# Kernel optimization log

Hardware: AMD Instinct MI355X
Metric: run time of the kernel (lower is better)

The kernel has to match this reference:

```python
import jax, jax.numpy as jnp
import numpy as np

D_MODEL = 1440; D_INNER = 2880; D_STATE = 128; HEADDIM = 64; NHEADS = 45
D_CONV = 4; NLAYERS = 32; VOCAB = 256; CHUNK = 128
D_XBC = D_INNER + 2 * D_STATE          # 3136 conv channels
D_PROJ = 2 * D_INNER + 2 * D_STATE + NHEADS  # 6061 in_proj width
EPS = 1e-5

def silu(x):
    return x * jax.nn.sigmoid(x)

def segsum(x):
    # x: (..., T) -> (..., T, T); out[i, j] = sum_{j < k <= i} x[k], -inf above diagonal
    T = x.shape[-1]
    xe = jnp.broadcast_to(x[..., None], (*x.shape, T))
    lower = jnp.tril(jnp.ones((T, T), bool), -1)
    cs = jnp.cumsum(jnp.where(lower, xe, 0.0), axis=-2)
    return jnp.where(jnp.tril(jnp.ones((T, T), bool)), cs, -jnp.inf)

def ssd(X, A, B, C):
    # Chunked SSD (Mamba2 'ssd_minimal_discrete'). X:(b,l,h,p) pre-multiplied by dt,
    # A:(b,l,h) = dt * A_head, B/C:(b,l,n) (ngroups=1, shared across heads).
    b, l, h, p = X.shape
    n = B.shape[-1]
    c = l // CHUNK
    Xc = X.reshape(b, c, CHUNK, h, p)
    Ac = A.reshape(b, c, CHUNK, h).transpose(0, 3, 1, 2)      # (b,h,c,q)
    Bc = B.reshape(b, c, CHUNK, n)
    Cc = C.reshape(b, c, CHUNK, n)
    A_cs = jnp.cumsum(Ac, axis=-1)                            # (b,h,c,q)
    L = jnp.exp(segsum(Ac))                                   # (b,h,c,q,q) intra-chunk decay
    Y_diag = jnp.einsum('bcln,bcsn,bhcls,bcshp->bclhp', Cc, Bc, L, Xc)
    decay_states = jnp.exp(A_cs[..., -1:] - A_cs)             # (b,h,c,q)
    states = jnp.einsum('bcln,bhcl,bclhp->bchpn', Bc, decay_states, Xc)
    A_last = jnp.pad(A_cs[..., -1], ((0, 0), (0, 0), (1, 0)))  # (b,h,c+1)
    decay_chunk = jnp.exp(segsum(A_last))                     # (b,h,c+1,c+1)
    states = jnp.concatenate([jnp.zeros_like(states[:, :1]), states], axis=1)
    states = jnp.einsum('bhzc,bchpn->bzhpn', decay_chunk, states)[:, :-1]  # (b,c,h,p,n)
    Y_off = jnp.einsum('bcln,bchpn,bhcl->bclhp', Cc, states, jnp.exp(A_cs))
    return (Y_diag + Y_off).reshape(b, l, h, p)

def mamba2_block(h, p):
    Win, conv_w, conv_b, dt_bias, A_log, Dp, norm_w, Wout = p
    b, l, _ = h.shape
    zxbcdt = h @ Win                                           # (b,l,6061)
    z = zxbcdt[..., :D_INNER]
    xBC = zxbcdt[..., D_INNER:D_INNER + D_XBC]
    dt = jax.nn.softplus(zxbcdt[..., -NHEADS:] + dt_bias)      # (b,l,H)
    # causal depthwise conv over time, kernel 4
    xp = jnp.pad(xBC, ((0, 0), (D_CONV - 1, 0), (0, 0))).transpose(0, 2, 1)  # (b,C,l+3)
    xBC = jax.lax.conv_general_dilated(xp, conv_w[:, None, :], (1,), 'VALID',
            feature_group_count=D_XBC, dimension_numbers=('NCH', 'OIH', 'NCH'))
    xBC = silu(xBC.transpose(0, 2, 1) + conv_b)                # (b,l,3136)
    x = xBC[..., :D_INNER].reshape(b, l, NHEADS, HEADDIM)
    B = xBC[..., D_INNER:D_INNER + D_STATE]
    C = xBC[..., D_INNER + D_STATE:]
    A = -jnp.exp(A_log)                                        # (H,)
    y = ssd(x * dt[..., None], dt * A, B, C)
    y = y + x * Dp[None, None, :, None]                        # D skip (on raw x)
    y = y.reshape(b, l, D_INNER) * silu(z)                     # gate, then RMSNormGated
    y = y * jax.lax.rsqrt(jnp.mean(y * y, -1, keepdims=True) + EPS) * norm_w
    return y @ Wout

def setup_inputs() -> dict:
    key = jax.random.key(0)
    ks = jax.random.split(key, 8)
    b, l = 2, 2048
    def nrm(k, shape, s=0.02):
        return jax.random.normal(k, shape, jnp.float32) * s
    tokens = jax.random.randint(ks[0], (b, l), 0, VOCAB)
    embed = nrm(ks[1], (VOCAB, D_MODEL))
    Win = nrm(ks[2], (NLAYERS, D_MODEL, D_PROJ))
    conv_w = nrm(ks[3], (NLAYERS, D_XBC, D_CONV), 0.2)
    conv_b = jnp.zeros((NLAYERS, D_XBC), jnp.float32)
    dtv = jnp.exp(jax.random.uniform(ks[4], (NLAYERS, NHEADS)) * (np.log(0.1) - np.log(1e-3)) + np.log(1e-3))
    dt_bias = dtv + jnp.log(-jnp.expm1(-dtv))                  # inverse softplus
    A_log = jnp.log(jax.random.uniform(ks[5], (NLAYERS, NHEADS), minval=1.0, maxval=16.0))
    Dp = jnp.ones((NLAYERS, NHEADS), jnp.float32)
    norm_w = jnp.ones((NLAYERS, D_INNER), jnp.float32)
    Wout = nrm(ks[6], (NLAYERS, D_INNER, D_MODEL))
    final_norm_w = jnp.ones((D_MODEL,), jnp.float32)
    return {'tokens': tokens, 'embed': embed, 'Win': Win, 'conv_w': conv_w,
            'conv_b': conv_b, 'dt_bias': dt_bias, 'A_log': A_log, 'Dp': Dp,
            'norm_w': norm_w, 'Wout': Wout, 'final_norm_w': final_norm_w}

def reference(tokens, embed, Win, conv_w, conv_b, dt_bias, A_log, Dp, norm_w, Wout, final_norm_w):
    h = embed[tokens]                                          # (b,l,d)
    layer_params = (Win, conv_w, conv_b, dt_bias, A_log, Dp, norm_w, Wout)
    def step(carry, p):
        return carry + mamba2_block(carry, p), None
    h, _ = jax.lax.scan(jax.checkpoint(step), h, layer_params)
    h = h * jax.lax.rsqrt(jnp.mean(h * h, -1, keepdims=True) + EPS) * final_norm_w
    return h @ embed.T                                         # tied head -> (b,l,256)
```

## Files before the change

kernel.cpp:

```cpp
#include <hip/hip_runtime.h>
#include <hip/hip_bf16.h>
#include <math.h>

#define NLAYERS 32
#define DM 1440
#define DI 2880
#define DSTATE 128
#define HD 64
#define NH 45
#define VOCABSZ 256
#define CHUNK 128
#define DXBC 3136
#define DPROJ 6061
#define BB 2
#define LL 2048
#define ROWS (BB*LL)
#define NCH (LL/CHUNK)
#define ZXS 6144
#define STR 136
#define STR2 68

typedef __attribute__((ext_vector_type(8))) short bf16x8;
typedef __attribute__((ext_vector_type(4))) float f32x4;
typedef unsigned short us;

__device__ __forceinline__ float sigmoidf_(float x){ return 1.0f/(1.0f+__expf(-x)); }
__device__ __forceinline__ us f2b(float f){
  unsigned int u = __float_as_uint(f);
  return (us)((u + 0x7FFFu + ((u>>16)&1u)) >> 16);
}
__device__ __forceinline__ float b2f(us s){
  return __uint_as_float(((unsigned int)s)<<16);
}
__device__ __forceinline__ void split2(float v, us* ph, us* pl){
  us h = f2b(v);
  *ph = h;
  *pl = f2b(v - b2f(h));
}
__device__ __forceinline__ void gl2lds16(const us* g, us* l){
  __builtin_amdgcn_global_load_lds((const __attribute__((address_space(1))) unsigned int*)g,
                                   (__attribute__((address_space(3))) unsigned int*)l, 16, 0, 0);
}
#define MFMA(a,b,c) __builtin_amdgcn_mfma_f32_16x16x32_bf16(a,b,c,0,0,0)

__global__ void k_embed(const int* __restrict__ tok, const float* __restrict__ emb, float* __restrict__ h){
  int idx = blockIdx.x*256 + threadIdx.x;
  if (idx >= ROWS*DM) return;
  int row = idx / DM, d = idx - row*DM;
  h[idx] = emb[tok[row]*DM + d];
}

__global__ void k_split_rows(const float* __restrict__ src, us* __restrict__ dh,
                             us* __restrict__ dl, int ncols){
  size_t e = ((size_t)blockIdx.x*256 + threadIdx.x)*8;
  const float* s = src + e;
  bf16x8 oh, ol;
  #pragma unroll
  for (int j=0;j<8;j++){
    float v = s[j];
    us hh = f2b(v);
    ((us*)&oh)[j] = hh;
    ((us*)&ol)[j] = f2b(v - b2f(hh));
  }
  *(bf16x8*)(dh + e) = oh;
  *(bf16x8*)(dl + e) = ol;
}

__global__ void k_transcast_sp(const float* __restrict__ W, us* __restrict__ WTh,
                               us* __restrict__ WTl, int K, int N){
  __shared__ float t[32][65];
  int tid = threadIdx.x;
  int n0 = blockIdx.x*64, k0 = blockIdx.y*32;
  #pragma unroll
  for (int i=0;i<8;i++){
    int e = i*256 + tid;
    int r = e >> 6, cc = e & 63;
    int n = n0 + cc;
    t[r][cc] = (n < N) ? W[(size_t)(k0+r)*N + n] : 0.f;
  }
  __syncthreads();
  int nrow = tid >> 2, kseg = (tid & 3)*8;
  bf16x8 oh, ol;
  #pragma unroll
  for (int j=0;j<8;j++){
    float v = t[kseg+j][nrow];
    us hh = f2b(v);
    ((us*)&oh)[j] = hh;
    ((us*)&ol)[j] = f2b(v - b2f(hh));
  }
  *(bf16x8*)(WTh + (size_t)(n0+nrow)*K + k0 + kseg) = oh;
  *(bf16x8*)(WTl + (size_t)(n0+nrow)*K + k0 + kseg) = ol;
}

template<bool ACC, bool SPL>
__global__ __launch_bounds__(256) void k_gemm_sp(const us* __restrict__ Ah, const us* __restrict__ Al,
      const us* __restrict__ Bh, const us* __restrict__ Bl, float* __restrict__ C,
      int K, int ldc, int N, int nbx, us* __restrict__ Oh, us* __restrict__ Ol){
  __shared__ __align__(16) us sAh[4096], sAl[4096], sBh[4096], sBl[4096];
  int nwg = gridDim.x;
  int q = nwg >> 3;
  int bid = blockIdx.x;
  int wg = (bid & 7)*q + (bid >> 3);
  int grp = wg / (4*nbx);
  int rem = wg - grp*4*nbx;
  int by = grp*4 + (rem & 3);
  int bx = rem >> 2;
  int m0 = by*128, n0 = bx*128;
  int tid = threadIdx.x;
  int lane = tid & 63, wid = tid >> 6;
  int wr = wid >> 1, wc = wid & 1;
  int r4 = lane >> 2, c4 = (lane & 3)*8;
  int fr = lane & 15, fk = (lane >> 4)*8;
  f32x4 acc[4][4];
  #pragma unroll
  for (int i=0;i<4;i++)
    #pragma unroll
    for (int j=0;j<4;j++) acc[i][j] = (f32x4){0.f,0.f,0.f,0.f};
  for (int kt = 0; kt < K; kt += 32){
    __syncthreads();
    size_t ra0 = (size_t)(m0 + wid*16     + r4)*K + kt + c4;
    size_t ra1 = (size_t)(m0 + (wid+4)*16 + r4)*K + kt + c4;
    size_t rb0 = (size_t)(n0 + wid*16     + r4)*K + kt + c4;
    size_t rb1 = (size_t)(n0 + (wid+4)*16 + r4)*K + kt + c4;
    gl2lds16(Ah + ra0, sAh + wid*512);
    gl2lds16(Ah + ra1, sAh + (wid+4)*512);
    gl2lds16(Al + ra0, sAl + wid*512);
    gl2lds16(Al + ra1, sAl + (wid+4)*512);
    gl2lds16(Bh + rb0, sBh + wid*512);
    gl2lds16(Bh + rb1, sBh + (wid+4)*512);
    gl2lds16(Bl + rb0, sBl + wid*512);
    gl2lds16(Bl + rb1, sBl + (wid+4)*512);
    __syncthreads();
    bf16x8 ah[4], al[4], bh[4], bl[4];
    #pragma unroll
    for (int i=0;i<4;i++){
      int ro = (wr*64 + i*16 + fr)*32 + fk;
      int co = (wc*64 + i*16 + fr)*32 + fk;
      ah[i] = *(const bf16x8*)(sAh + ro);
      al[i] = *(const bf16x8*)(sAl + ro);
      bh[i] = *(const bf16x8*)(sBh + co);
      bl[i] = *(const bf16x8*)(sBl + co);
    }
    #pragma unroll
    for (int i=0;i<4;i++)
      #pragma unroll
      for (int j=0;j<4;j++){
        acc[i][j] = MFMA(ah[i], bh[j], acc[i][j]);
        acc[i][j] = MFMA(ah[i], bl[j], acc[i][j]);
        acc[i][j] = MFMA(al[i], bh[j], acc[i][j]);
      }
  }
  int orow = (lane>>4)*4, ocol = lane & 15;
  #pragma unroll
  for (int i=0;i<4;i++)
    #pragma unroll
    for (int j=0;j<4;j++)
      #pragma unroll
      for (int r=0;r<4;r++){
        int col = n0 + wc*64 + j*16 + ocol;
        if (col < N){
          size_t off = (size_t)(m0 + wr*64 + i*16 + orow + r)*ldc + col;
          float v = acc[i][j][r] + (ACC ? C[off] : 0.f);
          C[off] = v;
          if (SPL) split2(v, &Oh[off], &Ol[off]);
        }
      }
}

__global__ __launch_bounds__(256) void k_conv2(const float* __restrict__ zx, const float* __restrict__ cw,
                        const float* __restrict__ cb, us* __restrict__ xbh, us* __restrict__ xbl){
  int ch = blockIdx.x*256 + threadIdx.x;
  if (ch >= DXBC) return;
  int l0 = blockIdx.y * 128;
  int b = blockIdx.z;
  float w0 = cw[ch*4+0], w1 = cw[ch*4+1], w2 = cw[ch*4+2], w3 = cw[ch*4+3];
  float bias = cb[ch];
  float x0=0.f, x1=0.f, x2=0.f;
  if (l0-3 >= 0) x0 = zx[(size_t)(b*LL + l0-3)*ZXS + DI + ch];
  if (l0-2 >= 0) x1 = zx[(size_t)(b*LL + l0-2)*ZXS + DI + ch];
  if (l0-1 >= 0) x2 = zx[(size_t)(b*LL + l0-1)*ZXS + DI + ch];
  for (int l = l0; l < l0+128; ++l){
    float x3 = zx[(size_t)(b*LL + l)*ZXS + DI + ch];
    float s = bias + w0*x0 + w1*x1 + w2*x2 + w3*x3;
    float v = s * sigmoidf_(s);
    size_t off = (size_t)(b*LL + l)*DXBC + ch;
    split2(v, &xbh[off], &xbl[off]);
    x0 = x1; x1 = x2; x2 = x3;
  }
}

__global__ void k_dt(const float* __restrict__ zx, const float* __restrict__ dtb_in, float* __restrict__ dt){
  int idx = blockIdx.x*256+threadIdx.x;
  if (idx >= ROWS*NH) return;
  int row = idx / NH, hh = idx - row*NH;
  float v = zx[(size_t)row*ZXS + (DI+DXBC) + hh] + dtb_in[hh];
  dt[idx] = (v > 20.f) ? v : log1pf(expf(v));
}

__global__ __launch_bounds__(256) void k_sraw(const us* __restrict__ xbh, const us* __restrict__ xbl,
                                              float* __restrict__ Sraw){
  __shared__ __align__(16) us sCh[128*STR], sCl[128*STR], sB2h[128*STR], sB2l[128*STR];
  int tid = threadIdx.x;
  int c = blockIdx.x, b = blockIdx.y;
  int t0 = b*LL + c*CHUNK;
  #pragma unroll
  for (int i=0;i<8;i++){
    int e = i*256 + tid;
    int l = e >> 4, seg = (e & 15)*8;
    size_t oc = (size_t)(t0+l)*DXBC + DI + DSTATE + seg;
    size_t ob = (size_t)(t0+l)*DXBC + DI + seg;
    *(bf16x8*)(sCh + l*STR + seg) = *(const bf16x8*)(xbh + oc);
    *(bf16x8*)(sCl + l*STR + seg) = *(const bf16x8*)(xbl + oc);
    *(bf16x8*)(sB2h + l*STR + seg) = *(const bf16x8*)(xbh + ob);
    *(bf16x8*)(sB2l + l*STR + seg) = *(const bf16x8*)(xbl + ob);
  }
  __syncthreads();
  int lane = tid & 63, wid = tid >> 6;
  int wbase = wid*32;
  int fr = lane & 15, fk = (lane>>4)*8;
  int orow = (lane>>4)*4;
  f32x4 accS[2][8];
  #pragma unroll
  for (int m=0;m<2;m++)
    #pragma unroll
    for (int j=0;j<8;j++) accS[m][j] = (f32x4){0.f,0.f,0.f,0.f};
  #pragma unroll
  for (int ks=0; ks<4; ++ks){
    int ko = ks*32 + fk;
    bf16x8 a0h = *(const bf16x8*)(sCh + (wbase+fr)*STR + ko);
    bf16x8 a0l = *(const bf16x8*)(sCl + (wbase+fr)*STR + ko);
    bf16x8 a1h = *(const bf16x8*)(sCh + (wbase+16+fr)*STR + ko);
    bf16x8 a1l = *(const bf16x8*)(sCl + (wbase+16+fr)*STR + ko);
    #pragma unroll
    for (int j=0;j<8;j++){
      bf16x8 bh = *(const bf16x8*)(sB2h + (j*16+fr)*STR + ko);
      bf16x8 bl = *(const bf16x8*)(sB2l + (j*16+fr)*STR + ko);
      accS[0][j] = MFMA(a0h, bh, accS[0][j]);
      accS[0][j] = MFMA(a0h, bl, accS[0][j]);
      accS[0][j] = MFMA(a0l, bh, accS[0][j]);
      accS[1][j] = MFMA(a1h, bh, accS[1][j]);
      accS[1][j] = MFMA(a1h, bl, accS[1][j]);
      accS[1][j] = MFMA(a1l, bh, accS[1][j]);
    }
  }
  size_t sbase = ((size_t)(b*NCH + c))*16384;
  #pragma unroll
  for (int m=0;m<2;m++)
    #pragma unroll
    for (int j=0;j<8;j++)
      #pragma unroll
      for (int r=0;r<4;r++){
        int l = wbase + m*16 + orow + r;
        int s = j*16 + fr;
        Sraw[sbase + l*128 + s] = accS[m][j][r];
      }
}

__global__ __launch_bounds__(256) void k_ssd_state_sp(const us* __restrict__ xbh, const us* __restrict__ xbl,
    const float* __restrict__ dtb, const float* __restrict__ Alog,
    float* __restrict__ acs, us* __restrict__ cst_h, us* __restrict__ cst_l){
  __shared__ __align__(16) us sBTh[64*STR], sBTl[64*STR];
  __shared__ __align__(16) us sXTh[64*STR], sXTl[64*STR];
  __shared__ float sAcs[128];
  __shared__ float sDt[128];
  int tid = threadIdx.x;
  int hh = blockIdx.x, c = blockIdx.y, b = blockIdx.z;
  int t0 = b*LL + c*CHUNK;
  float A_h = -__expf(Alog[hh]);
  if (tid < 128){
    float d = dtb[(size_t)(t0+tid)*NH + hh];
    sDt[tid] = d;
    sAcs[tid] = d * A_h;
  }
  __syncthreads();
  if (tid < 64){
    float v = sAcs[tid], w = sAcs[64+tid];
    #pragma unroll
    for (int off=1; off<64; off<<=1){
      float tv = __shfl_up(v, off, 64);
      float tw = __shfl_up(w, off, 64);
      if (tid >= off){ v += tv; w += tw; }
    }
    float tot = __shfl(v, 63, 64);
    sAcs[tid] = v;
    sAcs[64+tid] = w + tot;
  }
  __syncthreads();
  if (tid < 128) acs[(size_t)(t0+tid)*NH + hh] = sAcs[tid];
  float alast = sAcs[127];
  #pragma unroll 8
  for (int i=0;i<32;i++){
    int e = i*256 + tid;
    int l = e >> 6, p = e & 63;
    size_t off = (size_t)(t0+l)*DXBC + hh*HD + p;
    float v = (b2f(xbh[off]) + b2f(xbl[off])) * sDt[l] * __expf(alast - sAcs[l]);
    split2(v, &sXTh[p*STR+l], &sXTl[p*STR+l]);
  }
  int lane = tid & 63, wid = tid >> 6;
  int fr = lane & 15, fk = (lane>>4)*8;
  f32x4 acc[8];
  #pragma unroll
  for (int j=0;j<8;j++) acc[j] = (f32x4){0.f,0.f,0.f,0.f};
  #pragma unroll
  for (int nh=0; nh<2; ++nh){
    __syncthreads();
    #pragma unroll 8
    for (int i=0;i<32;i++){
      int e = i*256 + tid;
      int l = e >> 6, n = e & 63;
      size_t off = (size_t)(t0+l)*DXBC + DI + nh*64 + n;
      sBTh[n*STR+l] = xbh[off];
      sBTl[n*STR+l] = xbl[off];
    }
    __syncthreads();
    #pragma unroll
    for (int ks=0; ks<4; ks++){
      bf16x8 ah = *(const bf16x8*)(sXTh + (wid*16 + fr)*STR + ks*32 + fk);
      bf16x8 al = *(const bf16x8*)(sXTl + (wid*16 + fr)*STR + ks*32 + fk);
      #pragma unroll
      for (int j=0;j<4;j++){
        bf16x8 bh = *(const bf16x8*)(sBTh + (j*16 + fr)*STR + ks*32 + fk);
        bf16x8 bl = *(const bf16x8*)(sBTl + (j*16 + fr)*STR + ks*32 + fk);
        acc[nh*4+j] = MFMA(ah, bh, acc[nh*4+j]);
        acc[nh*4+j] = MFMA(ah, bl, acc[nh*4+j]);
        acc[nh*4+j] = MFMA(al, bh, acc[nh*4+j]);
      }
    }
  }
  size_t cbase = (((size_t)(b*NCH + c)*NH) + hh)*8192;
  int orow = (lane>>4)*4;
  #pragma unroll
  for (int jj=0;jj<8;jj++)
    #pragma unroll
    for (int r=0;r<4;r++){
      int p = wid*16 + orow + r;
      int n = (jj>>2)*64 + (jj&3)*16 + fr;
      split2(acc[jj][r], &cst_h[cbase + p*128 + n], &cst_l[cbase + p*128 + n]);
    }
}

__global__ __launch_bounds__(256) void k_ssd_scan2(const float* __restrict__ acs,
      us* __restrict__ cst_h, us* __restrict__ cst_l){
  int tid = threadIdx.x;
  int hh = blockIdx.x, b = blockIdx.y, z = blockIdx.z;
  int base_e = z*1024;
  float P[4];
  #pragma unroll
  for (int i=0;i<4;i++) P[i] = 0.f;
  for (int c=0;c<NCH;c++){
    size_t base = (((size_t)(b*NCH + c)*NH) + hh)*8192 + base_e;
    float dec = __expf(acs[(size_t)(b*LL + c*CHUNK + CHUNK-1)*NH + hh]);
    #pragma unroll
    for (int i=0;i<4;i++){
      size_t e = base + i*256 + tid;
      float tmp = b2f(cst_h[e]) + b2f(cst_l[e]);
      split2(P[i], &cst_h[e], &cst_l[e]);
      P[i] = dec*P[i] + tmp;
    }
  }
}

__global__ __launch_bounds__(512) void k_ssd_y_sp(const us* __restrict__ xbh, const us* __restrict__ xbl,
    const float* __restrict__ dtb, const float* __restrict__ acs,
    const us* __restrict__ cst_h, const us* __restrict__ cst_l,
    const float* __restrict__ Sraw, float* __restrict__ Yf){
  __shared__ __align__(16) us smem[26112];
  __shared__ float sAcs[128];
  __shared__ float sDt[128];
  us* sCh = smem;          us* sCl = smem + 8704;
  us* sPh = smem + 17408;  us* sPl = smem + 21760;
  us* sSh = smem;          us* sSl = smem + 8704;
  us* sXh = smem + 17408;  us* sXl = smem + 21760;

  int tid = threadIdx.x;
  int hh = blockIdx.x, c = blockIdx.y, b = blockIdx.z;
  int t0 = b*LL + c*CHUNK;
  if (tid < 128){
    sAcs[tid] = acs[(size_t)(t0+tid)*NH + hh];
    sDt[tid]  = dtb[(size_t)(t0+tid)*NH + hh];
  }
  int lane = tid & 63, wid = tid >> 6;
  int wbase = wid*16;
  int fr = lane & 15, fk = (lane>>4)*8;
  int orow = (lane>>4)*4;
  size_t cbase = (((size_t)(b*NCH + c)*NH) + hh)*8192;
  size_t sbase = ((size_t)(b*NCH + c))*16384;

  f32x4 accU[4], accD[4];
  #pragma unroll
  for (int j=0;j<4;j++){
    accU[j] = (f32x4){0.f,0.f,0.f,0.f};
    accD[j] = (f32x4){0.f,0.f,0.f,0.f};
  }

  #pragma unroll
  for (int nt=0; nt<2; ++nt){
    int nb = nt*64;
    __syncthreads();
    #pragma unroll 8
    for (int i=0;i<16;i++){
      int e = i*512 + tid;
      int l = e >> 6, nn = e & 63;
      size_t oc = (size_t)(t0+l)*DXBC + DI + DSTATE + nb + nn;
      sCh[l*STR2+nn] = xbh[oc];  sCl[l*STR2+nn] = xbl[oc];
    }
    #pragma unroll 8
    for (int i=0;i<8;i++){
      int e = i*512 + tid;
      int p = e >> 6, nn = e & 63;
      sPh[p*STR2+nn] = cst_h[cbase + p*128 + nb + nn];
      sPl[p*STR2+nn] = cst_l[cbase + p*128 + nb + nn];
    }
    __syncthreads();
    #pragma unroll
    for (int ks=0; ks<2; ++ks){
      int ko = ks*32 + fk;
      bf16x8 a0h = *(const bf16x8*)(sCh + (wbase+fr)*STR2 + ko);
      bf16x8 a0l = *(const bf16x8*)(sCl + (wbase+fr)*STR2 + ko);
      #pragma unroll
      for (int j=0;j<4;j++){
        bf16x8 ph = *(const bf16x8*)(sPh + (j*16+fr)*STR2 + ko);
        bf16x8 pl = *(const bf16x8*)(sPl + (j*16+fr)*STR2 + ko);
        accU[j] = MFMA(a0h, ph, accU[j]);
        accU[j] = MFMA(a0h, pl, accU[j]);
        accU[j] = MFMA(a0l, ph, accU[j]);
      }
    }
  }

  #pragma unroll
  for (int sh=0; sh<2; ++sh){
    __syncthreads();
    #pragma unroll 8
    for (int i=0;i<16;i++){
      int e = i*512 + tid;
      int l = e >> 6, ss = e & 63;
      int s = sh*64 + ss;
      float raw = Sraw[sbase + l*128 + s];
      float v = (s <= l) ? raw*__expf(sAcs[l]-sAcs[s])*sDt[s] : 0.f;
      split2(v, &sSh[l*STR2+ss], &sSl[l*STR2+ss]);
    }
    #pragma unroll 8
    for (int i=0;i<8;i++){
      int e = i*512 + tid;
      int sl = e >> 6, p = e & 63;
      size_t off = (size_t)(t0 + sh*64 + sl)*DXBC + hh*HD + p;
      sXh[p*STR2 + sl] = xbh[off];
      sXl[p*STR2 + sl] = xbl[off];
    }
    __syncthreads();
    #pragma unroll
    for (int ks=0; ks<2; ++ks){
      int ko = ks*32 + fk;
      bf16x8 a0h = *(const bf16x8*)(sSh + (wbase+fr)*STR2 + ko);
      bf16x8 a0l = *(const bf16x8*)(sSl + (wbase+fr)*STR2 + ko);
      #pragma unroll
      for (int j=0;j<4;j++){
        bf16x8 xh = *(const bf16x8*)(sXh + (j*16+fr)*STR2 + ko);
        bf16x8 xl = *(const bf16x8*)(sXl + (j*16+fr)*STR2 + ko);
        accD[j] = MFMA(a0h, xh, accD[j]);
        accD[j] = MFMA(a0h, xl, accD[j]);
        accD[j] = MFMA(a0l, xh, accD[j]);
      }
    }
  }
  #pragma unroll
  for (int r=0;r<4;r++){
    int l = wbase + orow + r;
    float ea = __expf(sAcs[l]);
    #pragma unroll
    for (int j=0;j<4;j++)
      Yf[(size_t)(t0+l)*DI + hh*HD + j*16 + fr] = accD[j][r] + ea*accU[j][r];
  }
}

__global__ __launch_bounds__(256) void k_gatenorm(const float* __restrict__ Yf,
                           const us* __restrict__ xbh, const us* __restrict__ xbl,
                           const float* __restrict__ zx, const float* __restrict__ Dp_l,
                           const float* __restrict__ nw, us* __restrict__ yh, us* __restrict__ yl){
  __shared__ float red[4];
  __shared__ float stot;
  int row = blockIdx.x;
  int tid = threadIdx.x;
  float yv_[12];
  float ss = 0.f;
  #pragma unroll
  for (int i=0;i<12;i++){
    int d = tid + i*256;
    if (d < DI){
      size_t xo = (size_t)row*DXBC + d;
      float xv = b2f(xbh[xo]) + b2f(xbl[xo]);
      float yv = Yf[(size_t)row*DI + d] + xv * Dp_l[d >> 6];
      float zv = zx[(size_t)row*ZXS + d];
      yv *= zv * sigmoidf_(zv);
      yv_[i] = yv;
      ss += yv*yv;
    } else yv_[i] = 0.f;
  }
  #pragma unroll
  for (int off=32; off>0; off>>=1) ss += __shfl_down(ss, off, 64);
  int lane = tid & 63, wid = tid >> 6;
  if (lane == 0) red[wid] = ss;
  __syncthreads();
  if (tid == 0) stot = red[0]+red[1]+red[2]+red[3];
  __syncthreads();
  float rs = rsqrtf(stot / (float)DI + 1e-5f);
  #pragma unroll
  for (int i=0;i<12;i++){
    int d = tid + i*256;
    if (d < DI){
      float v = yv_[i] * rs * nw[d];
      split2(v, &yh[(size_t)row*DI + d], &yl[(size_t)row*DI + d]);
    }
  }
}

__global__ __launch_bounds__(256) void k_finalnorm(const float* __restrict__ h, const float* __restrict__ fnw,
                            us* __restrict__ oh, us* __restrict__ ol){
  __shared__ float red[4];
  __shared__ float stot;
  int row = blockIdx.x;
  int tid = threadIdx.x;
  float v_[6];
  float ss = 0.f;
  #pragma unroll
  for (int i=0;i<6;i++){
    int d = tid + i*256;
    if (d < DM){ v_[i] = h[(size_t)row*DM + d]; ss += v_[i]*v_[i]; }
    else v_[i] = 0.f;
  }
  #pragma unroll
  for (int off=32; off>0; off>>=1) ss += __shfl_down(ss, off, 64);
  int lane = tid & 63, wid = tid >> 6;
  if (lane == 0) red[wid] = ss;
  __syncthreads();
  if (tid == 0) stot = red[0]+red[1]+red[2]+red[3];
  __syncthreads();
  float rs = rsqrtf(stot / (float)DM + 1e-5f);
  #pragma unroll
  for (int i=0;i<6;i++){
    int d = tid + i*256;
    if (d < DM){
      float v = v_[i] * rs * fnw[d];
      split2(v, &oh[(size_t)row*DM + d], &ol[(size_t)row*DM + d]);
    }
  }
}

extern "C" void kernel_launch(void* const* d_in, const int* in_sizes, int n_in,
                              void* d_out, int out_size, void* d_ws, size_t ws_size,
                              hipStream_t stream){
  const int*   tok   = (const int*)d_in[0];
  const float* emb   = (const float*)d_in[1];
  const float* Win   = (const float*)d_in[2];
  const float* convw = (const float*)d_in[3];
  const float* convb = (const float*)d_in[4];
  const float* dtbias= (const float*)d_in[5];
  const float* Alog  = (const float*)d_in[6];
  const float* Dp    = (const float*)d_in[7];
  const float* normw = (const float*)d_in[8];
  const float* Wout  = (const float*)d_in[9];
  const float* fnw   = (const float*)d_in[10];

  float* ws = (float*)d_ws;
  float* h    = ws;
  float* zx   = ws + 5898240;
  us*    xbh  = (us*)(ws + 31064064);
  us*    xbl  = (us*)(ws + 37486592);
  us*    hp_h = (us*)(ws + 31064064);
  us*    hp_l = (us*)(ws + 34013184);
  float* dtb  = ws + 43909120;
  float* acs  = ws + 44093440;
  float* Yf   = ws + 44277760;
  us* wbuf_h  = (us*)(ws + 44277760);
  us* wbuf_l  = (us*)(ws + 48701440);
  us* cst_h   = (us*)(ws + 56074240);
  us* cst_l   = (us*)(ws + 61972480);
  us* ab_h    = (us*)(ws + 56074240);
  us* ab_l    = (us*)(ws + 61972480);
  float* Sraw = ws + 67870720;

  k_embed<<<(ROWS*DM+255)/256, 256, 0, stream>>>(tok, emb, h);
  k_split_rows<<<2880, 256, 0, stream>>>(h, hp_h, hp_l, DM);
  for (int lyr=0; lyr<NLAYERS; ++lyr){
    k_transcast_sp<<<dim3(ZXS/64, DM/32), 256, 0, stream>>>(Win + (size_t)lyr*DM*DPROJ, wbuf_h, wbuf_l, DM, DPROJ);
    k_gemm_sp<false,false><<<(ZXS/128)*(ROWS/128), 256, 0, stream>>>(hp_h, hp_l, wbuf_h, wbuf_l, zx, DM, ZXS, ZXS, ZXS/128, nullptr, nullptr);
    k_conv2<<<dim3(13, 16, BB), 256, 0, stream>>>(
        zx, convw + (size_t)lyr*DXBC*4, convb + (size_t)lyr*DXBC, xbh, xbl);
    k_dt<<<(ROWS*NH+255)/256, 256, 0, stream>>>(zx, dtbias + lyr*NH, dtb);
    k_sraw<<<dim3(NCH, BB), 256, 0, stream>>>(xbh, xbl, Sraw);
    k_ssd_state_sp<<<dim3(NH, NCH, BB), 256, 0, stream>>>(xbh, xbl, dtb, Alog + lyr*NH, acs, cst_h, cst_l);
    k_ssd_scan2<<<dim3(NH, BB, 8), 256, 0, stream>>>(acs, cst_h, cst_l);
    k_ssd_y_sp<<<dim3(NH, NCH, BB), 512, 0, stream>>>(xbh, xbl, dtb, acs, cst_h, cst_l, Sraw, Yf);
    k_gatenorm<<<ROWS, 256, 0, stream>>>(Yf, xbh, xbl, zx, Dp + lyr*NH, normw + (size_t)lyr*DI, ab_h, ab_l);
    k_transcast_sp<<<dim3(1536/64, DI/32), 256, 0, stream>>>(Wout + (size_t)lyr*DI*DM, wbuf_h, wbuf_l, DI, DM);
    k_gemm_sp<true,true><<<(1536/128)*(ROWS/128), 256, 0, stream>>>(ab_h, ab_l, wbuf_h, wbuf_l, h, DI, DM, DM, 1536/128, hp_h, hp_l);
  }
  k_finalnorm<<<ROWS, 256, 0, stream>>>(h, fnw, ab_h, ab_l);
  k_split_rows<<<180, 256, 0, stream>>>(emb, wbuf_h, wbuf_l, DM);
  k_gemm_sp<false,false><<<(VOCABSZ/128)*(ROWS/128), 256, 0, stream>>>(ab_h, ab_l, wbuf_h, wbuf_l, (float*)d_out, DM, VOCABSZ, VOCABSZ, VOCABSZ/128, nullptr, nullptr);
}
```

Measured before the change: 22.80 ms.

## Fold split-bf16 in_proj into single concatenated-K GEMM with 256x256 pipelined tiles

```diff
diff --git a/kernel.cpp b/kernel.cpp
--- a/kernel.cpp
+++ b/kernel.cpp
@@ -17,6 +17,7 @@
 #define ROWS (BB*LL)
 #define NCH (LL/CHUNK)
 #define ZXS 6144
+#define KC 4352
 #define STR 136
 #define STR2 68
 
@@ -66,8 +67,34 @@
   *(bf16x8*)(dl + e) = ol;
 }
 
-__global__ void k_transcast_sp(const float* __restrict__ W, us* __restrict__ WTh,
-                               us* __restrict__ WTl, int K, int N){
+__global__ void k_split3_rows(const float* __restrict__ src, us* __restrict__ A2){
+  int bid = blockIdx.x;
+  int tid = threadIdx.x;
+  if (bid >= 2880){
+    int e2 = (bid-2880)*256 + tid;
+    int row = e2 >> 2, seg = (e2 & 3)*8;
+    bf16x8 z = (bf16x8){0,0,0,0,0,0,0,0};
+    *(bf16x8*)(A2 + (size_t)row*KC + 4320 + seg) = z;
+    return;
+  }
+  size_t e = ((size_t)bid*256 + tid)*8;
+  int row = (int)(e / DM), col = (int)(e - (size_t)row*DM);
+  const float* s = src + e;
+  bf16x8 oh, ol;
+  #pragma unroll
+  for (int j=0;j<8;j++){
+    float v = s[j];
+    us hh = f2b(v);
+    ((us*)&oh)[j] = hh;
+    ((us*)&ol)[j] = f2b(v - b2f(hh));
+  }
+  us* base = A2 + (size_t)row*KC + col;
+  *(bf16x8*)(base) = oh;
+  *(bf16x8*)(base + 1440) = ol;
+  *(bf16x8*)(base + 2880) = oh;
+}
+
+__global__ void k_transcast3(const float* __restrict__ W, us* __restrict__ B2, int N){
   __shared__ float t[32][65];
   int tid = threadIdx.x;
   int n0 = blockIdx.x*64, k0 = blockIdx.y*32;
@@ -88,14 +115,119 @@
     ((us*)&oh)[j] = hh;
     ((us*)&ol)[j] = f2b(v - b2f(hh));
   }
+  us* base = B2 + (size_t)(n0+nrow)*KC + k0 + kseg;
+  *(bf16x8*)(base) = oh;
+  *(bf16x8*)(base + 1440) = oh;
+  *(bf16x8*)(base + 2880) = ol;
+}
+
+__global__ void k_transcast_sp(const float* __restrict__ W, us* __restrict__ WTh,
+                               us* __restrict__ WTl, int K, int N){
+  __shared__ float t[32][65];
+  int tid = threadIdx.x;
+  int n0 = blockIdx.x*64, k0 = blockIdx.y*32;
+  #pragma unroll
+  for (int i=0;i<8;i++){
+    int e = i*256 + tid;
+    int r = e >> 6, cc = e & 63;
+    int n = n0 + cc;
+    t[r][cc] = (n < N) ? W[(size_t)(k0+r)*N + n] : 0.f;
+  }
+  __syncthreads();
+  int nrow = tid >> 2, kseg = (tid & 3)*8;
+  bf16x8 oh, ol;
+  #pragma unroll
+  for (int j=0;j<8;j++){
+    float v = t[kseg+j][nrow];
+    us hh = f2b(v);
+    ((us*)&oh)[j] = hh;
+    ((us*)&ol)[j] = f2b(v - b2f(hh));
+  }
   *(bf16x8*)(WTh + (size_t)(n0+nrow)*K + k0 + kseg) = oh;
   *(bf16x8*)(WTl + (size_t)(n0+nrow)*K + k0 + kseg) = ol;
 }
 
-template<bool ACC, bool SPL>
+__global__ __launch_bounds__(512) void k_gemm8(const us* __restrict__ A, const us* __restrict__ B,
+      float* __restrict__ C, int ldc, int nbx){
+  __shared__ __align__(16) us lds[65536];
+  const int nt = KC/32;
+  int nwg = gridDim.x;
+  int bid = blockIdx.x;
+  int q = nwg >> 3;
+  int wg = (bid & 7)*q + (bid >> 3);
+  int grp = wg / (4*nbx);
+  int rem = wg - grp*4*nbx;
+  int by = grp*4 + (rem & 3);
+  int bx = rem >> 2;
+  int m0 = by*256, n0 = bx*256;
+  int tid = threadIdx.x;
+  int lane = tid & 63, wid = tid >> 6;
+  int wr = wid >> 2, wc = wid & 3;
+  int fr = lane & 15, fk4 = lane >> 4;
+  int srow = lane >> 2, sslot = lane & 3;
+  f32x4 acc[8][4];
+  #pragma unroll
+  for (int m=0;m<8;m++)
+    #pragma unroll
+    for (int n=0;n<4;n++) acc[m][n] = (f32x4){0.f,0.f,0.f,0.f};
+
+  #define STAGE(T) {                                                                   \
+    int b_ = (T) & 3; int kb_ = (T)*32;                                                \
+    _Pragma("unroll")                                                                  \
+    for (int c_=0;c_<4;c_++){                                                          \
+      int rl_ = ((c_&1)*128) + wid*16 + srow;                                          \
+      int seg_ = sslot ^ ((rl_>>1)&3);                                                 \
+      const us* src_ = (c_>=2) ? (B + (size_t)(n0+rl_)*KC + kb_ + seg_*8)              \
+                               : (A + (size_t)(m0+rl_)*KC + kb_ + seg_*8);             \
+      gl2lds16(src_, lds + b_*16384 + c_*4096 + wid*512);                              \
+    }                                                                                  \
+  }
+
+  STAGE(0); STAGE(1); STAGE(2);
+  for (int t=0; t<nt; ++t){
+    int remt = nt-1-t;
+    if (remt >= 2)      asm volatile("s_waitcnt vmcnt(8)" ::: "memory");
+    else if (remt == 1) asm volatile("s_waitcnt vmcnt(4)" ::: "memory");
+    else                asm volatile("s_waitcnt vmcnt(0)" ::: "memory");
+    asm volatile("s_barrier" ::: "memory");
+    if (t+3 < nt) STAGE(t+3);
+    int b = t & 3;
+    const us* bufA = lds + b*16384;
+    const us* bufB = lds + b*16384 + 8192;
+    bf16x8 af[8], bfv[4];
+    #pragma unroll
+    for (int m=0;m<8;m++){
+      int rl = wr*128 + m*16 + fr;
+      af[m] = *(const bf16x8*)(bufA + rl*32 + (fk4 ^ ((rl>>1)&3))*8);
+    }
+    #pragma unroll
+    for (int n=0;n<4;n++){
+      int rl = wc*64 + n*16 + fr;
+      bfv[n] = *(const bf16x8*)(bufB + rl*32 + (fk4 ^ ((rl>>1)&3))*8);
+    }
+    __builtin_amdgcn_s_setprio(1);
+    #pragma unroll
+    for (int m=0;m<8;m++)
+      #pragma unroll
+      for (int n=0;n<4;n++)
+        acc[m][n] = MFMA(af[m], bfv[n], acc[m][n]);
+    __builtin_amdgcn_s_setprio(0);
+  }
+  #undef STAGE
+  int orow = (lane>>4)*4, ocol = lane & 15;
+  #pragma unroll
+  for (int m=0;m<8;m++)
+    #pragma unroll
+    for (int n=0;n<4;n++)
+      #pragma unroll
+      for (int r=0;r<4;r++)
+        C[(size_t)(m0 + wr*128 + m*16 + orow + r)*ldc + n0 + wc*64 + n*16 + ocol] = acc[m][n][r];
+}
+
+template<bool ACC, int SPLMODE>
 __global__ __launch_bounds__(256) void k_gemm_sp(const us* __restrict__ Ah, const us* __restrict__ Al,
       const us* __restrict__ Bh, const us* __restrict__ Bl, float* __restrict__ C,
-      int K, int ldc, int N, int nbx, us* __restrict__ Oh, us* __restrict__ Ol){
+      int K, int ldc, int N, int nbx, us* __restrict__ A2){
   __shared__ __align__(16) us sAh[4096], sAl[4096], sBh[4096], sBl[4096];
   int nwg = gridDim.x;
   int q = nwg >> 3;
@@ -159,10 +291,16 @@
       for (int r=0;r<4;r++){
         int col = n0 + wc*64 + j*16 + ocol;
         if (col < N){
-          size_t off = (size_t)(m0 + wr*64 + i*16 + orow + r)*ldc + col;
+          int row = m0 + wr*64 + i*16 + orow + r;
+          size_t off = (size_t)row*ldc + col;
           float v = acc[i][j][r] + (ACC ? C[off] : 0.f);
           C[off] = v;
-          if (SPL) split2(v, &Oh[off], &Ol[off]);
+          if (SPLMODE == 2){
+            us hh = f2b(v);
+            us ll = f2b(v - b2f(hh));
+            us* base = A2 + (size_t)row*KC + col;
+            base[0] = hh; base[1440] = ll; base[2880] = hh;
+          }
         }
       }
 }
@@ -392,7 +530,6 @@
     accU[j] = (f32x4){0.f,0.f,0.f,0.f};
     accD[j] = (f32x4){0.f,0.f,0.f,0.f};
   }
-
   #pragma unroll
   for (int nt=0; nt<2; ++nt){
     int nb = nt*64;
@@ -427,7 +564,6 @@
       }
     }
   }
-
   #pragma unroll
   for (int sh=0; sh<2; ++sh){
     __syncthreads();
@@ -567,8 +703,6 @@
   float* zx   = ws + 5898240;
   us*    xbh  = (us*)(ws + 31064064);
   us*    xbl  = (us*)(ws + 37486592);
-  us*    hp_h = (us*)(ws + 31064064);
-  us*    hp_l = (us*)(ws + 34013184);
   float* dtb  = ws + 43909120;
   float* acs  = ws + 44093440;
   float* Yf   = ws + 44277760;
@@ -579,12 +713,14 @@
   us* ab_h    = (us*)(ws + 56074240);
   us* ab_l    = (us*)(ws + 61972480);
   float* Sraw = ws + 67870720;
+  us*    A2   = (us*)(ws + 68395008);
+  us*    B2   = (us*)(ws + 77307904);
 
   k_embed<<<(ROWS*DM+255)/256, 256, 0, stream>>>(tok, emb, h);
-  k_split_rows<<<2880, 256, 0, stream>>>(h, hp_h, hp_l, DM);
+  k_split3_rows<<<2944, 256, 0, stream>>>(h, A2);
   for (int lyr=0; lyr<NLAYERS; ++lyr){
-    k_transcast_sp<<<dim3(ZXS/64, DM/32), 256, 0, stream>>>(Win + (size_t)lyr*DM*DPROJ, wbuf_h, wbuf_l, DM, DPROJ);
-    k_gemm_sp<false,false><<<(ZXS/128)*(ROWS/128), 256, 0, stream>>>(hp_h, hp_l, wbuf_h, wbuf_l, zx, DM, ZXS, ZXS, ZXS/128, nullptr, nullptr);
+    k_transcast3<<<dim3(ZXS/64, DM/32), 256, 0, stream>>>(Win + (size_t)lyr*DM*DPROJ, B2, DPROJ);
+    k_gemm8<<<(ZXS/256)*(ROWS/256), 512, 0, stream>>>(A2, B2, zx, ZXS, ZXS/256);
     k_conv2<<<dim3(13, 16, BB), 256, 0, stream>>>(
         zx, convw + (size_t)lyr*DXBC*4, convb + (size_t)lyr*DXBC, xbh, xbl);
     k_dt<<<(ROWS*NH+255)/256, 256, 0, stream>>>(zx, dtbias + lyr*NH, dtb);
@@ -594,9 +730,9 @@
     k_ssd_y_sp<<<dim3(NH, NCH, BB), 512, 0, stream>>>(xbh, xbl, dtb, acs, cst_h, cst_l, Sraw, Yf);
     k_gatenorm<<<ROWS, 256, 0, stream>>>(Yf, xbh, xbl, zx, Dp + lyr*NH, normw + (size_t)lyr*DI, ab_h, ab_l);
     k_transcast_sp<<<dim3(1536/64, DI/32), 256, 0, stream>>>(Wout + (size_t)lyr*DI*DM, wbuf_h, wbuf_l, DI, DM);
-    k_gemm_sp<true,true><<<(1536/128)*(ROWS/128), 256, 0, stream>>>(ab_h, ab_l, wbuf_h, wbuf_l, h, DI, DM, DM, 1536/128, hp_h, hp_l);
+    k_gemm_sp<true,2><<<(1536/128)*(ROWS/128), 256, 0, stream>>>(ab_h, ab_l, wbuf_h, wbuf_l, h, DI, DM, DM, 1536/128, A2);
   }
   k_finalnorm<<<ROWS, 256, 0, stream>>>(h, fnw, ab_h, ab_l);
   k_split_rows<<<180, 256, 0, stream>>>(emb, wbuf_h, wbuf_l, DM);
-  k_gemm_sp<false,false><<<(VOCABSZ/128)*(ROWS/128), 256, 0, stream>>>(ab_h, ab_l, wbuf_h, wbuf_l, (float*)d_out, DM, VOCABSZ, VOCABSZ, VOCABSZ/128, nullptr, nullptr);
-}
+  k_gemm_sp<false,0><<<(VOCABSZ/128)*(ROWS/128), 256, 0, stream>>>(ab_h, ab_l, wbuf_h, wbuf_l, (float*)d_out, DM, VOCABSZ, VOCABSZ, VOCABSZ/128, nullptr);
+}
```

New measurement: 23.54 ms. 1.03x slower.
